# Performance work log

Measured on AMD Instinct MI355X. Metric: run time of the kernel, lower is better.

The kernel has to match this reference:

```python
import jax, jax.numpy as jnp
import numpy as np
import math

DIM = 512
WINDOW = 4
TOPK = 8


def setup_inputs() -> dict:
    key = jax.random.key(0)
    ks = jax.random.split(key, 14)
    B, N, D = 4, 4096, DIM
    s = 0.02
    return {
        'mu':  jax.random.normal(ks[0], (B, N, D), jnp.float32),
        'Wq':  jax.random.normal(ks[1], (D, D), jnp.float32) * s,
        'bq':  jnp.zeros((D,), jnp.float32),
        'Wk':  jax.random.normal(ks[2], (D, D), jnp.float32) * s,
        'bk':  jnp.zeros((D,), jnp.float32),
        'Wv':  jax.random.normal(ks[3], (D, D), jnp.float32) * s,
        'bv':  jnp.zeros((D,), jnp.float32),
        'Wm1': jax.random.normal(ks[4], (2 * D, D), jnp.float32) * s,
        'bm1': jnp.zeros((D,), jnp.float32),
        'Wm2': jax.random.normal(ks[5], (D, D), jnp.float32) * s,
        'bm2': jnp.zeros((D,), jnp.float32),
        'Wo':  jax.random.normal(ks[6], (2 * D, D), jnp.float32) * s,
        'bo':  jnp.zeros((D,), jnp.float32),
    }


def reference(mu, Wq, bq, Wk, bk, Wv, bv, Wm1, bm1, Wm2, bm2, Wo, bo):
    B, N, D = mu.shape
    W = WINDOW
    # ---- local windowed message passing ----
    padded = jnp.pad(mu, ((0, 0), (W, 0), (0, 0)))  # left-pad seq with W zeros
    # neighbors[:, n, w-1] = mu[:, n-w] (zeros if n-w < 0); [B, N, W, D]
    neighbors = jnp.stack([padded[:, W - w:W - w + N, :] for w in range(1, W + 1)], axis=2)
    self_exp = jnp.broadcast_to(mu[:, :, None, :], neighbors.shape)
    h = jnp.concatenate([self_exp, neighbors], axis=-1)  # [B, N, W, 2D]
    h = jax.nn.silu(h @ Wm1 + bm1)
    local_msgs = (h @ Wm2 + bm2).mean(axis=2)  # [B, N, D]
    # ---- sparse causal global attention ----
    q = mu @ Wq + bq
    k = mu @ Wk + bk
    v = mu @ Wv + bv
    scores = jnp.einsum('bnd,bmd->bnm', q, k) * (1.0 / math.sqrt(D))
    causal = jnp.tril(jnp.ones((N, N), bool))
    scores = jnp.where(causal, scores, -jnp.inf)
    # top-k then softmax over kept entries == softmax over scatter(-inf elsewhere)
    topk_vals, topk_idx = jax.lax.top_k(scores, TOPK)  # [B, N, K]
    probs = jax.nn.softmax(topk_vals, axis=-1)
    bi = jnp.arange(B)[:, None, None]
    ni = jnp.arange(N)[None, :, None]
    attn = jnp.zeros_like(scores).at[bi, ni, topk_idx].set(probs)  # [B, N, N]
    global_msgs = jnp.einsum('bnm,bmd->bnd', attn, v)
    return jnp.concatenate([local_msgs, global_msgs], axis=-1) @ Wo + bo
```

## Files before the change

### kernel.cpp

```cpp
#include <hip/hip_runtime.h>
#include <math.h>

#define DIM 512
#define NSEQ 4096
#define BATCH 4
#define ROWS (BATCH * NSEQ)

typedef unsigned long long u64;
typedef unsigned int u32;
typedef unsigned short u16;
typedef __attribute__((ext_vector_type(8))) short bf16x8;
typedef __attribute__((ext_vector_type(4))) float f32x4;

typedef const __attribute__((address_space(1))) void* gas1;
typedef __attribute__((address_space(3))) void* las3;

__device__ __forceinline__ u32 to_bf16(float f) {
  u32 x = __float_as_uint(f);
  return (x + 0x7fffu + ((x >> 16) & 1u)) >> 16;
}
__device__ __forceinline__ u32 pk2(float a, float b) {
  return to_bf16(a) | (to_bf16(b) << 16);
}
__device__ __forceinline__ uint4 pk8(float4 a, float4 b) {
  return make_uint4(pk2(a.x, a.y), pk2(a.z, a.w), pk2(b.x, b.y), pk2(b.z, b.w));
}
__device__ __forceinline__ float bf2f(u32 lo16) {
  return __uint_as_float(lo16 << 16);
}

__device__ __forceinline__ void insert_top8(u64 (&a)[8], u64 key) {
  if (key <= a[7]) return;
  a[7] = key;
#pragma unroll
  for (int i = 7; i > 0; --i) {
    u64 x = a[i - 1], y = a[i];
    u64 hi = x > y ? x : y;
    u64 lo = x > y ? y : x;
    a[i - 1] = hi;
    a[i] = lo;
  }
}
template<int NN>
__device__ __forceinline__ void insert_topN(u64 (&a)[NN], u64 key) {
  if (key <= a[NN - 1]) return;
  a[NN - 1] = key;
#pragma unroll
  for (int i = NN - 1; i > 0; --i) {
    u64 x = a[i - 1], y = a[i];
    u64 hi = x > y ? x : y;
    u64 lo = x > y ? y : x;
    a[i - 1] = hi;
    a[i] = lo;
  }
}
__device__ __forceinline__ float decode_val(u64 key) {
  u32 ord = (u32)(key >> 32);
  u32 s = (ord & 0x80000000u) ? (ord ^ 0x80000000u) : ~ord;
  return __uint_as_float(s);
}
__device__ __forceinline__ u64 pack_key(float v, int m) {
  u32 sb = __float_as_uint(v);
  u32 ord = sb ^ ((sb >> 31) ? 0xFFFFFFFFu : 0x80000000u);
  return ((u64)ord << 32) | (u32)(~(u32)m);
}

__device__ __forceinline__ int fbal(int sub) {
  const int g = sub >> 5, i = sub & 31;
  return (g == 0) ? i : (g == 1) ? (63 - i) : (g == 2) ? (64 + i) : (127 - i);
}

__global__ __launch_bounds__(256) void gemm64qk(const float* __restrict__ mu,
                                                const float* __restrict__ Wq,
                                                const float* __restrict__ bq,
                                                const float* __restrict__ Wk,
                                                const float* __restrict__ bk,
                                                float* __restrict__ Q,
                                                float* __restrict__ Kf,
                                                u16* __restrict__ Kc,
                                                u16* __restrict__ Mu16) {
  __shared__ float As[16][132];
  __shared__ float Bs[16][144];
  const int tid = threadIdx.x;
  const int tx = tid & 15, ty = tid >> 4;
  const int bx = blockIdx.x;
  const bool isK = bx >= 4;
  const int n0 = (bx & 3) * 128;
  const int m0 = blockIdx.y * 128;
  const float* W = isK ? Wk : Wq;
  const float* bias = isK ? bk : bq;
  float* C = isK ? Kf : Q;
  const int arow = tid >> 1, ah8 = (tid & 1) * 8;
  const int bkk = tid >> 4, bslot = tid & 15;
  float acc[8][8] = {};
  for (int k0 = 0; k0 < DIM; k0 += 16) {
    float4 a0 = *(const float4*)(mu + (size_t)(m0 + arow) * DIM + (k0 + ah8));
    float4 a1 = *(const float4*)(mu + (size_t)(m0 + arow) * DIM + (k0 + ah8 + 4));
    float4 b0 = *(const float4*)(W + (size_t)(k0 + bkk) * DIM + (n0 + bslot * 8));
    float4 b1 = *(const float4*)(W + (size_t)(k0 + bkk) * DIM + (n0 + bslot * 8 + 4));
    if (bx == 0)
      *(uint4*)(Mu16 + (size_t)(m0 + arow) * DIM + k0 + ah8) = pk8(a0, a1);
    As[ah8 + 0][arow] = a0.x; As[ah8 + 1][arow] = a0.y;
    As[ah8 + 2][arow] = a0.z; As[ah8 + 3][arow] = a0.w;
    As[ah8 + 4][arow] = a1.x; As[ah8 + 5][arow] = a1.y;
    As[ah8 + 6][arow] = a1.z; As[ah8 + 7][arow] = a1.w;
    *(float4*)&Bs[bkk][bslot * 9] = b0;
    *(float4*)&Bs[bkk][bslot * 9 + 4] = b1;
    __syncthreads();
#pragma unroll
    for (int kk = 0; kk < 16; ++kk) {
      float4 av0 = *(const float4*)&As[kk][ty * 8];
      float4 av1 = *(const float4*)&As[kk][ty * 8 + 4];
      float4 bv0 = *(const float4*)&Bs[kk][tx * 9];
      float4 bv1 = *(const float4*)&Bs[kk][tx * 9 + 4];
      float a8[8] = {av0.x, av0.y, av0.z, av0.w, av1.x, av1.y, av1.z, av1.w};
      float b8[8] = {bv0.x, bv0.y, bv0.z, bv0.w, bv1.x, bv1.y, bv1.z, bv1.w};
#pragma unroll
      for (int i = 0; i < 8; ++i)
#pragma unroll
        for (int j = 0; j < 8; ++j)
          acc[i][j] = fmaf(a8[i], b8[j], acc[i][j]);
    }
    __syncthreads();
  }
  float4 bb0 = *(const float4*)(bias + n0 + tx * 8);
  float4 bb1 = *(const float4*)(bias + n0 + tx * 8 + 4);
#pragma unroll
  for (int i = 0; i < 8; ++i) {
    int row = m0 + ty * 8 + i;
#pragma unroll
    for (int jb = 0; jb < 2; ++jb) {
      int col = n0 + tx * 8 + jb * 4;
      float4 bb = jb ? bb1 : bb0;
      float4 o;
      o.x = acc[i][jb * 4 + 0] + bb.x;
      o.y = acc[i][jb * 4 + 1] + bb.y;
      o.z = acc[i][jb * 4 + 2] + bb.z;
      o.w = acc[i][jb * 4 + 3] + bb.w;
      *(float4*)(C + (size_t)row * DIM + col) = o;
      if (isK) {
        int batch = row >> 12, key = row & 4095;
        int kt = key >> 6, kl = key & 63;
        int chunk = col >> 5;
        size_t didx = ((size_t)batch << 21) +
                      ((size_t)((kt * 16 + chunk) * 64 + kl)) * 32 + (col & 31);
        *(uint2*)(Kc + didx) = make_uint2(pk2(o.x, o.y), pk2(o.z, o.w));
      }
    }
  }
}

__global__ __launch_bounds__(256) void wtrans7(const float* __restrict__ Wv,
                                               const float* __restrict__ Wm1,
                                               const float* __restrict__ Wm2,
                                               const float* __restrict__ Wo,
                                               u16* __restrict__ WT) {
  const size_t DD = (size_t)DIM * DIM;
  const int y = blockIdx.y;
  u16* dst = WT + (size_t)y * DD;
  int o = blockIdx.x * 256 + threadIdx.x;
  if (y == 6) {
    const float* s = Wm2 + (size_t)o * 4;
    ((uint2*)dst)[o] = make_uint2(pk2(s[0], s[1]), pk2(s[2], s[3]));
    return;
  }
  const float* src = (y == 0) ? Wv
                   : (y == 1) ? Wm1
                   : (y == 2) ? Wm1 + DD
                   : (y == 3) ? Wm2
                   : (y == 4) ? Wo
                              : Wo + DD;
  int n = o >> 7;
  int k0 = (o & 127) * 4;
  float a0 = src[(size_t)(k0 + 0) * DIM + n];
  float a1 = src[(size_t)(k0 + 1) * DIM + n];
  float a2 = src[(size_t)(k0 + 2) * DIM + n];
  float a3 = src[(size_t)(k0 + 3) * DIM + n];
  ((uint2*)dst)[(n << 7) + (k0 >> 2)] = make_uint2(pk2(a0, a1), pk2(a2, a3));
}

__global__ __launch_bounds__(256) void wtrans2(const float* __restrict__ Wcombf,
                                               const u16* __restrict__ WoBT,
                                               u16* __restrict__ WT2) {
  int o = blockIdx.x * 256 + threadIdx.x;
  int n = o >> 8;
  int k = (o & 255) * 4;
  if (k < 512) {
    float a0 = Wcombf[(size_t)(k + 0) * DIM + n];
    float a1 = Wcombf[(size_t)(k + 1) * DIM + n];
    float a2 = Wcombf[(size_t)(k + 2) * DIM + n];
    float a3 = Wcombf[(size_t)(k + 3) * DIM + n];
    *(uint2*)&WT2[(size_t)n * 1024 + k] = make_uint2(pk2(a0, a1), pk2(a2, a3));
  } else {
    *(uint2*)&WT2[(size_t)n * 1024 + k] = *(const uint2*)&WoBT[(size_t)n * 512 + (k - 512)];
  }
}

__global__ void bcomb_k(const float* __restrict__ bm2, const float* __restrict__ Wo,
                        const float* __restrict__ bo, float* __restrict__ bc) {
  int c = blockIdx.x * 256 + threadIdx.x;
  if (c >= DIM) return;
  float s = bo[c];
  for (int k = 0; k < DIM; ++k) s = fmaf(bm2[k], Wo[(size_t)k * DIM + c], s);
  bc[c] = s;
}

__global__ __launch_bounds__(256, 4) void gemmbf(const u16* __restrict__ A, int lda,
                                                 const u16* __restrict__ WT, int K,
                                                 const float* __restrict__ bias,
                                                 float* C, int ldc) {
  __shared__ u16 As[128 * 32];
  __shared__ u16 Bs[128 * 32];
  const int tid = threadIdx.x;
  const int n0 = blockIdx.x * 128;
  const int m0 = blockIdx.y * 128;
  const int l = tid & 63, lr = l & 15, lu = l >> 4;
  const int wid = tid >> 6, wr = wid >> 1, wc = wid & 1;
  const int lrow = l >> 2, lseg = (l & 3) * 8;
  f32x4 acc[4][4] = {};
  for (int k0 = 0; k0 < K; k0 += 32) {
    __syncthreads();
#pragma unroll
    for (int j = 0; j < 2; ++j) {
      int r0 = wid * 32 + j * 16;
      const u16* sa = A + (size_t)(m0 + r0 + lrow) * lda + k0 + lseg;
      const u16* sb = WT + (size_t)(n0 + r0 + lrow) * K + k0 + lseg;
      __builtin_amdgcn_global_load_lds((gas1)sa, (las3)&As[r0 * 32], 16, 0, 0);
      __builtin_amdgcn_global_load_lds((gas1)sb, (las3)&Bs[r0 * 32], 16, 0, 0);
    }
    __syncthreads();
    bf16x8 af[4], bf_[4];
#pragma unroll
    for (int fr = 0; fr < 4; ++fr) {
      int row = wr * 64 + fr * 16 + lr;
      af[fr] = *(const bf16x8*)&As[row * 32 + lu * 8];
    }
#pragma unroll
    for (int fc = 0; fc < 4; ++fc) {
      int col = wc * 64 + fc * 16 + lr;
      bf_[fc] = *(const bf16x8*)&Bs[col * 32 + lu * 8];
    }
#pragma unroll
    for (int fr = 0; fr < 4; ++fr)
#pragma unroll
      for (int fc = 0; fc < 4; ++fc)
        acc[fr][fc] = __builtin_amdgcn_mfma_f32_16x16x32_bf16(af[fr], bf_[fc], acc[fr][fc], 0, 0, 0);
  }
#pragma unroll
  for (int fr = 0; fr < 4; ++fr)
#pragma unroll
    for (int fc = 0; fc < 4; ++fc) {
      int col = n0 + wc * 64 + fc * 16 + lr;
      float bb = bias ? bias[col] : 0.f;
#pragma unroll
      for (int j = 0; j < 4; ++j) {
        int row = m0 + wr * 64 + fr * 16 + lu * 4 + j;
        C[(size_t)row * ldc + col] = acc[fr][fc][j] + bb;
      }
    }
}

__global__ __launch_bounds__(256, 4) void gemmbf_b16(const u16* __restrict__ A, int lda,
                                                     const u16* __restrict__ WT, int K,
                                                     const float* __restrict__ bias,
                                                     u16* Cb, int ldc) {
  __shared__ u16 As[128 * 32];
  __shared__ u16 Bs[128 * 32];
  const int tid = threadIdx.x;
  const int n0 = blockIdx.x * 128;
  const int m0 = blockIdx.y * 128;
  const int l = tid & 63, lr = l & 15, lu = l >> 4;
  const int wid = tid >> 6, wr = wid >> 1, wc = wid & 1;
  const int lrow = l >> 2, lseg = (l & 3) * 8;
  f32x4 acc[4][4] = {};
  for (int k0 = 0; k0 < K; k0 += 32) {
    __syncthreads();
#pragma unroll
    for (int j = 0; j < 2; ++j) {
      int r0 = wid * 32 + j * 16;
      const u16* sa = A + (size_t)(m0 + r0 + lrow) * lda + k0 + lseg;
      const u16* sb = WT + (size_t)(n0 + r0 + lrow) * K + k0 + lseg;
      __builtin_amdgcn_global_load_lds((gas1)sa, (las3)&As[r0 * 32], 16, 0, 0);
      __builtin_amdgcn_global_load_lds((gas1)sb, (las3)&Bs[r0 * 32], 16, 0, 0);
    }
    __syncthreads();
    bf16x8 af[4], bf_[4];
#pragma unroll
    for (int fr = 0; fr < 4; ++fr) {
      int row = wr * 64 + fr * 16 + lr;
      af[fr] = *(const bf16x8*)&As[row * 32 + lu * 8];
    }
#pragma unroll
    for (int fc = 0; fc < 4; ++fc) {
      int col = wc * 64 + fc * 16 + lr;
      bf_[fc] = *(const bf16x8*)&Bs[col * 32 + lu * 8];
    }
#pragma unroll
    for (int fr = 0; fr < 4; ++fr)
#pragma unroll
      for (int fc = 0; fc < 4; ++fc)
        acc[fr][fc] = __builtin_amdgcn_mfma_f32_16x16x32_bf16(af[fr], bf_[fc], acc[fr][fc], 0, 0, 0);
  }
#pragma unroll
  for (int fr = 0; fr < 4; ++fr)
#pragma unroll
    for (int fc = 0; fc < 4; ++fc) {
      int col = n0 + wc * 64 + fc * 16 + lr;
      float bb = bias ? bias[col] : 0.f;
#pragma unroll
      for (int j = 0; j < 4; ++j) {
        int row = m0 + wr * 64 + fr * 16 + lu * 4 + j;
        Cb[(size_t)row * ldc + col] = (u16)to_bf16(acc[fr][fc][j] + bb);
      }
    }
}

__global__ __launch_bounds__(256) void silu_combine(const u16* __restrict__ Pair,
                                                    const float* __restrict__ bm1,
                                                    u16* __restrict__ P16) {
  size_t idx = (size_t)blockIdx.x * 256 + threadIdx.x;
  int r = (int)(idx >> 7);
  int c4 = (int)(idx & 127);
  int n = r & (NSEQ - 1);
  uint2 av = *(const uint2*)&Pair[(size_t)r * 1024 + c4 * 4];
  const float4 bm = ((const float4*)bm1)[c4];
  float bx = bf2f(av.x & 0xffffu) + bm.x;
  float by = __uint_as_float(av.x & 0xffff0000u) + bm.y;
  float bz = bf2f(av.y & 0xffffu) + bm.z;
  float bw = __uint_as_float(av.y & 0xffff0000u) + bm.w;
  float sx = 0.f, sy = 0.f, sz = 0.f, sw = 0.f;
#pragma unroll
  for (int w = 1; w <= 4; ++w) {
    float ex = bx, ey = by, ez = bz, ew = bw;
    if (n >= w) {
      uint2 nb = *(const uint2*)&Pair[(size_t)(r - w) * 1024 + 512 + c4 * 4];
      ex += bf2f(nb.x & 0xffffu);
      ey += __uint_as_float(nb.x & 0xffff0000u);
      ez += bf2f(nb.y & 0xffffu);
      ew += __uint_as_float(nb.y & 0xffff0000u);
    }
    sx += ex / (1.f + expf(-ex));
    sy += ey / (1.f + expf(-ey));
    sz += ez / (1.f + expf(-ez));
    sw += ew / (1.f + expf(-ew));
  }
  *(uint2*)(P16 + (size_t)r * 1024 + c4 * 4) =
      make_uint2(pk2(0.25f * sx, 0.25f * sy), pk2(0.25f * sz, 0.25f * sw));
}

__global__ __launch_bounds__(256, 4) void attn_fused(const float* __restrict__ Qf,
                                                     const float* __restrict__ Kf,
                                                     const u16* __restrict__ Kc,
                                                     const u16* __restrict__ V16,
                                                     u16* __restrict__ P16) {
  __shared__ union UA {
    struct { u16 Qs[16 * 512]; u64 cand[256][8]; } s;
    float Qf32[16][512];
  } uA;
  __shared__ int cidx[16][16];
  __shared__ u64 exkey[16][16];
  __shared__ float psm[16][8];
  __shared__ int pidx[16][8];

  const int tid = threadIdx.x;
  const int bid = blockIdx.x;
  const int xcd = bid & 7;
  const int b = xcd >> 1;
  const int par = xcd & 1;
  const int sub = bid >> 3;
  const int qt = 2 * fbal(sub) + par;
  const int n0 = qt * 16;
  const size_t rb = (size_t)b * NSEQ;
  const float SCALE_F = 0.04419417382415922f;

  const int l = tid & 63, lr = l & 15, lu = l >> 4;
  const int wid = tid >> 6;
  const int mbase = lu * 4;

  {
    int row = tid >> 4, part = tid & 15;
    const float4* src = (const float4*)(Qf + ((rb + n0 + row) << 9));
#pragma unroll
    for (int c = 0; c < 4; ++c) {
      int slot = part * 4 + c;
      float4 x = src[slot * 2], y = src[slot * 2 + 1];
      *(uint4*)&uA.s.Qs[row * 512 + (slot ^ (row & 7)) * 8] = pk8(x, y);
    }
  }
  __syncthreads();

  u64 best[8] = {};
  const int nq = n0 + lr;

  const int nkt = (n0 + 16 + 63) >> 6;
  const int lo = (lr * 32) + lu * 8;
  for (int kt = wid; kt < nkt; kt += 4) {
    const int m0 = kt << 6;
    const u16* kb = Kc + ((size_t)b << 21) + (size_t)kt * 32768;
    f32x4 acc[4] = {};
    bf16x8 kcur[4], knxt[4];
#pragma unroll
    for (int fk = 0; fk < 4; ++fk)
      kcur[fk] = *(const bf16x8*)(kb + fk * 512 + lo);
#pragma unroll
    for (int ks = 0; ks < 16; ++ks) {
      if (ks < 15) {
        const u16* cb = kb + (ks + 1) * 2048;
#pragma unroll
        for (int fk = 0; fk < 4; ++fk)
          knxt[fk] = *(const bf16x8*)(cb + fk * 512 + lo);
      }
      bf16x8 qf = *(const bf16x8*)&uA.s.Qs[lr * 512 + ((ks * 4 + lu) ^ (lr & 7)) * 8];
      __builtin_amdgcn_s_setprio(1);
#pragma unroll
      for (int fk = 0; fk < 4; ++fk)
        acc[fk] = __builtin_amdgcn_mfma_f32_16x16x32_bf16(kcur[fk], qf, acc[fk], 0, 0, 0);
      __builtin_amdgcn_s_setprio(0);
      if (ks < 15) {
#pragma unroll
        for (int fk = 0; fk < 4; ++fk) kcur[fk] = knxt[fk];
      }
    }
    if (m0 + 63 <= n0) {
#pragma unroll
      for (int fk = 0; fk < 4; ++fk)
#pragma unroll
        for (int j = 0; j < 4; ++j)
          insert_top8(best, pack_key(acc[fk][j], m0 + fk * 16 + mbase + j));
    } else {
#pragma unroll
      for (int fk = 0; fk < 4; ++fk)
#pragma unroll
        for (int j = 0; j < 4; ++j) {
          int m = m0 + fk * 16 + mbase + j;
          if (m <= nq) insert_top8(best, pack_key(acc[fk][j], m));
        }
    }
  }

  __syncthreads();
#pragma unroll
  for (int i = 0; i < 8; ++i) uA.s.cand[tid][i] = best[i];
  __syncthreads();

  if (tid < 16) {
    u64 mb[16] = {};
    for (int w = 0; w < 4; ++w)
      for (int u = 0; u < 4; ++u) {
        const u64* cl = uA.s.cand[w * 64 + u * 16 + tid];
#pragma unroll
        for (int i = 0; i < 8; ++i) insert_topN<16>(mb, cl[i]);
      }
#pragma unroll
    for (int i = 0; i < 16; ++i)
      cidx[tid][i] = (mb[i] != 0ULL) ? (int)(~(u32)mb[i]) : -1;
  }
  __syncthreads();

  {
    int row = tid >> 4, seg = tid & 15;
    const float4* src = (const float4*)(Qf + ((rb + n0 + row) << 9));
    float4* dst = (float4*)&uA.Qf32[row][0];
#pragma unroll
    for (int c = 0; c < 8; ++c) dst[seg * 8 + c] = src[seg * 8 + c];
  }
  __syncthreads();

  {
    const int g = tid >> 2;
    const int lsub = tid & 3;
    const int qi = g >> 2;
    const int cblk = g & 3;
    const float4* q4 = (const float4*)&uA.Qf32[qi][0];
#pragma unroll
    for (int cc = 0; cc < 4; ++cc) {
      int c = cblk * 4 + cc;
      int ci = cidx[qi][c];
      float4 p = make_float4(0.f, 0.f, 0.f, 0.f);
      if (ci >= 0) {
        const float4* k4 = (const float4*)(Kf + ((rb + ci) << 9));
#pragma unroll 8
        for (int t = 0; t < 32; ++t) {
          float4 kv = k4[4 * t + lsub];
          float4 qv = q4[4 * t + lsub];
          p.x = fmaf(kv.x, qv.x, p.x);
          p.y = fmaf(kv.y, qv.y, p.y);
          p.z = fmaf(kv.z, qv.z, p.z);
          p.w = fmaf(kv.w, qv.w, p.w);
        }
      }
      p.x += __shfl_xor(p.x, 2);
      p.y += __shfl_xor(p.y, 2);
      p.z += __shfl_xor(p.z, 2);
      p.w += __shfl_xor(p.w, 2);
      p.x += __shfl_xor(p.x, 1);
      p.y += __shfl_xor(p.y, 1);
      p.z += __shfl_xor(p.z, 1);
      p.w += __shfl_xor(p.w, 1);
      float rx = p.x + p.z;
      float ry = p.y + p.w;
      float r = rx + ry;
      if (lsub == 0)
        exkey[qi][c] = (ci >= 0) ? pack_key(r * SCALE_F, ci) : 0ULL;
    }
  }
  __syncthreads();

  if (tid < 16) {
    u64 mb[8] = {};
#pragma unroll
    for (int t2 = 0; t2 < 16; ++t2) insert_top8(mb, exkey[tid][t2]);
    float vmax = decode_val(mb[0]);
    float e[8];
#pragma unroll
    for (int i = 0; i < 8; ++i)
      e[i] = (mb[i] != 0ULL) ? expf(decode_val(mb[i]) - vmax) : 0.f;
    float s01 = e[0] + e[1], s23 = e[2] + e[3];
    float s45 = e[4] + e[5], s67 = e[6] + e[7];
    float ssum = (s01 + s23) + (s45 + s67);
#pragma unroll
    for (int i = 0; i < 8; ++i) {
      psm[tid][i] = e[i] / ssum;
      pidx[tid][i] = (mb[i] != 0ULL) ? (int)(~(u32)mb[i]) : 0;
    }
  }
  __syncthreads();

  {
    const int qi = tid >> 4, seg = tid & 15;
    float pp[8];
    int ix[8];
#pragma unroll
    for (int i = 0; i < 8; ++i) { pp[i] = psm[qi][i]; ix[i] = pidx[qi][i]; }
    u16* Gb = P16 + ((size_t)(rb + n0 + qi)) * 1024 + 512 + seg * 32;
#pragma unroll
    for (int it = 0; it < 8; ++it) {
      float4 a = make_float4(0.f, 0.f, 0.f, 0.f);
#pragma unroll
      for (int i = 0; i < 8; ++i) {
        uint2 vv = *(const uint2*)(V16 + ((size_t)(rb + ix[i])) * 512 + seg * 32 + it * 4);
        a.x = fmaf(pp[i], bf2f(vv.x & 0xffffu), a.x);
        a.y = fmaf(pp[i], __uint_as_float(vv.x & 0xffff0000u), a.y);
        a.z = fmaf(pp[i], bf2f(vv.y & 0xffffu), a.z);
        a.w = fmaf(pp[i], __uint_as_float(vv.y & 0xffff0000u), a.w);
      }
      *(uint2*)(Gb + it * 4) = make_uint2(pk2(a.x, a.y), pk2(a.z, a.w));
    }
  }
}

extern "C" void kernel_launch(void* const* d_in, const int* in_sizes, int n_in,
                              void* d_out, int out_size, void* d_ws, size_t ws_size,
                              hipStream_t stream) {
  const float* mu = (const float*)d_in[0];
  const float* Wq = (const float*)d_in[1];
  const float* bq = (const float*)d_in[2];
  const float* Wk = (const float*)d_in[3];
  const float* bk = (const float*)d_in[4];
  const float* Wv = (const float*)d_in[5];
  const float* bv = (const float*)d_in[6];
  const float* Wm1 = (const float*)d_in[7];
  const float* bm1 = (const float*)d_in[8];
  const float* Wm2 = (const float*)d_in[9];
  const float* bm2 = (const float*)d_in[10];
  const float* Wo = (const float*)d_in[11];
  const float* bo = (const float*)d_in[12];
  float* out = (float*)d_out;

  float* ws = (float*)d_ws;
  const size_t RD = (size_t)ROWS * DIM;
  const size_t DD = (size_t)DIM * DIM;
  float* X1 = ws;
  float* X2 = X1 + RD;
  u16* P16 = (u16*)(X2 + RD);
  u16* Pair = P16 + RD * 2;
  u16* V16 = Pair + RD * 2;
  u16* Kc = V16 + RD;
  u16* WT = Kc + RD;
  u16* WvT = WT;
  u16* Wm1aT = WT + DD;
  u16* WoTT = WT + 4 * DD;
  u16* WoBT = WT + 5 * DD;
  u16* Wm216 = WT + 6 * DD;
  u16* WT2 = WT + 7 * DD;
  float* Wcombf = (float*)(WT2 + (size_t)512 * 1024);
  float* bcomb = Wcombf + DD;
  u16* Mu16 = (u16*)(bcomb + 512);

  dim3 blk(256);
  dim3 gqk(8, ROWS / 128);
  dim3 gbf(DIM / 128, ROWS / 128);
  dim3 gbf2(2 * DIM / 128, ROWS / 128);

  wtrans7<<<dim3(256, 7), blk, 0, stream>>>(Wv, Wm1, Wm2, Wo, WT);
  gemmbf<<<dim3(4, 4), blk, 0, stream>>>(Wm216, 512, WoTT, 512, (const float*)nullptr, Wcombf, 512);
  bcomb_k<<<dim3(2), blk, 0, stream>>>(bm2, Wo, bo, bcomb);
  wtrans2<<<dim3(512), blk, 0, stream>>>(Wcombf, WoBT, WT2);

  gemm64qk<<<gqk, blk, 0, stream>>>(mu, Wq, bq, Wk, bk, X1, X2, Kc, Mu16);

  gemmbf_b16<<<gbf, blk, 0, stream>>>(Mu16, 512, WvT, 512, bv, V16, 512);

  attn_fused<<<dim3(1024), blk, 0, stream>>>(X1, X2, Kc, V16, P16);

  gemmbf_b16<<<gbf2, blk, 0, stream>>>(Mu16, 512, Wm1aT, 512, (const float*)nullptr, Pair, 1024);
  silu_combine<<<dim3(ROWS * 128 / 256), blk, 0, stream>>>(Pair, bm1, P16);

  gemmbf<<<dim3(4, 128), blk, 0, stream>>>(P16, 1024, WT2, 1024, bcomb, out, 512);
}
```

Baseline: 635.1 us.

## Pre-transpose mu and double-buffer QK GEMM with direct global-to-LDS loads

Adds a transpose kernel that writes mu in column-major fp32 form and emits the bf16 copy, taking that work out of the QK GEMM. The fp32 QK GEMM then uses global_load_lds to fill double-buffered LDS tiles, so the next k-tile loads while the current one is computed, replacing register staging and scattered LDS stores. This costs an extra pass over mu (a 32 MB read and a 32 MB write) and extra workspace. The LDS padding is removed, which may add bank conflicts.

New measurement: 635.1 us. No clear change (-0.0%).

```diff
diff --git a/kernel.cpp b/kernel.cpp
--- a/kernel.cpp
+++ b/kernel.cpp
@@ -70,17 +70,35 @@
   return (g == 0) ? i : (g == 1) ? (63 - i) : (g == 2) ? (64 + i) : (127 - i);
 }
 
-__global__ __launch_bounds__(256) void gemm64qk(const float* __restrict__ mu,
+__global__ __launch_bounds__(256) void mutrans(const float* __restrict__ mu,
+                                               float* __restrict__ muT,
+                                               u16* __restrict__ Mu16) {
+  __shared__ float t[32][33];
+  const int kb = blockIdx.x * 32;
+  const int rb = blockIdx.y * 32;
+  const int tx = threadIdx.x & 31, ty = threadIdx.x >> 5;
+#pragma unroll
+  for (int i = 0; i < 32; i += 8) {
+    float v = mu[(size_t)(rb + ty + i) * DIM + kb + tx];
+    t[ty + i][tx] = v;
+    Mu16[(size_t)(rb + ty + i) * DIM + kb + tx] = (u16)to_bf16(v);
+  }
+  __syncthreads();
+#pragma unroll
+  for (int i = 0; i < 32; i += 8)
+    muT[(size_t)(kb + ty + i) * ROWS + rb + tx] = t[tx][ty + i];
+}
+
+__global__ __launch_bounds__(256) void gemm64qk(const float* __restrict__ muT,
                                                 const float* __restrict__ Wq,
                                                 const float* __restrict__ bq,
                                                 const float* __restrict__ Wk,
                                                 const float* __restrict__ bk,
                                                 float* __restrict__ Q,
                                                 float* __restrict__ Kf,
-                                                u16* __restrict__ Kc,
-                                                u16* __restrict__ Mu16) {
-  __shared__ float As[16][132];
-  __shared__ float Bs[16][144];
+                                                u16* __restrict__ Kc) {
+  __shared__ float As[2][16][128];
+  __shared__ float Bs[2][16][128];
   const int tid = threadIdx.x;
   const int tx = tid & 15, ty = tid >> 4;
   const int bx = blockIdx.x;
@@ -90,29 +108,34 @@
   const float* W = isK ? Wk : Wq;
   const float* bias = isK ? bk : bq;
   float* C = isK ? Kf : Q;
-  const int arow = tid >> 1, ah8 = (tid & 1) * 8;
-  const int bkk = tid >> 4, bslot = tid & 15;
+  const int wid = tid >> 6, l = tid & 63;
+  const int lrow = l >> 5;
+  const int lcol = (l & 31) * 4;
+
+#define QK_STAGE(buf, k0)                                                      \
+  {                                                                            \
+    _Pragma("unroll")                                                          \
+    for (int j = 0; j < 2; ++j) {                                              \
+      int kk0 = wid * 4 + j * 2;                                               \
+      const float* sa = muT + (size_t)((k0) + kk0 + lrow) * ROWS + m0 + lcol;  \
+      const float* sb = W + (size_t)((k0) + kk0 + lrow) * DIM + n0 + lcol;     \
+      __builtin_amdgcn_global_load_lds((gas1)sa, (las3)&As[buf][kk0][0], 16, 0, 0); \
+      __builtin_amdgcn_global_load_lds((gas1)sb, (las3)&Bs[buf][kk0][0], 16, 0, 0); \
+    }                                                                          \
+  }
+
   float acc[8][8] = {};
-  for (int k0 = 0; k0 < DIM; k0 += 16) {
-    float4 a0 = *(const float4*)(mu + (size_t)(m0 + arow) * DIM + (k0 + ah8));
-    float4 a1 = *(const float4*)(mu + (size_t)(m0 + arow) * DIM + (k0 + ah8 + 4));
-    float4 b0 = *(const float4*)(W + (size_t)(k0 + bkk) * DIM + (n0 + bslot * 8));
-    float4 b1 = *(const float4*)(W + (size_t)(k0 + bkk) * DIM + (n0 + bslot * 8 + 4));
-    if (bx == 0)
-      *(uint4*)(Mu16 + (size_t)(m0 + arow) * DIM + k0 + ah8) = pk8(a0, a1);
-    As[ah8 + 0][arow] = a0.x; As[ah8 + 1][arow] = a0.y;
-    As[ah8 + 2][arow] = a0.z; As[ah8 + 3][arow] = a0.w;
-    As[ah8 + 4][arow] = a1.x; As[ah8 + 5][arow] = a1.y;
-    As[ah8 + 6][arow] = a1.z; As[ah8 + 7][arow] = a1.w;
-    *(float4*)&Bs[bkk][bslot * 9] = b0;
-    *(float4*)&Bs[bkk][bslot * 9 + 4] = b1;
-    __syncthreads();
+  QK_STAGE(0, 0);
+  __syncthreads();
+  for (int t = 0; t < 32; ++t) {
+    const int buf = t & 1;
+    if (t < 31) QK_STAGE(buf ^ 1, (t + 1) * 16);
 #pragma unroll
     for (int kk = 0; kk < 16; ++kk) {
-      float4 av0 = *(const float4*)&As[kk][ty * 8];
-      float4 av1 = *(const float4*)&As[kk][ty * 8 + 4];
-      float4 bv0 = *(const float4*)&Bs[kk][tx * 9];
-      float4 bv1 = *(const float4*)&Bs[kk][tx * 9 + 4];
+      float4 av0 = *(const float4*)&As[buf][kk][ty * 8];
+      float4 av1 = *(const float4*)&As[buf][kk][ty * 8 + 4];
+      float4 bv0 = *(const float4*)&Bs[buf][kk][tx * 8];
+      float4 bv1 = *(const float4*)&Bs[buf][kk][tx * 8 + 4];
       float a8[8] = {av0.x, av0.y, av0.z, av0.w, av1.x, av1.y, av1.z, av1.w};
       float b8[8] = {bv0.x, bv0.y, bv0.z, bv0.w, bv1.x, bv1.y, bv1.z, bv1.w};
 #pragma unroll
@@ -123,6 +146,8 @@
     }
     __syncthreads();
   }
+#undef QK_STAGE
+
   float4 bb0 = *(const float4*)(bias + n0 + tx * 8);
   float4 bb1 = *(const float4*)(bias + n0 + tx * 8 + 4);
 #pragma unroll
@@ -586,6 +611,7 @@
   float* Wcombf = (float*)(WT2 + (size_t)512 * 1024);
   float* bcomb = Wcombf + DD;
   u16* Mu16 = (u16*)(bcomb + 512);
+  float* MuT = (float*)(Mu16 + RD);
 
   dim3 blk(256);
   dim3 gqk(8, ROWS / 128);
@@ -597,7 +623,9 @@
   bcomb_k<<<dim3(2), blk, 0, stream>>>(bm2, Wo, bo, bcomb);
   wtrans2<<<dim3(512), blk, 0, stream>>>(Wcombf, WoBT, WT2);
 
-  gemm64qk<<<gqk, blk, 0, stream>>>(mu, Wq, bq, Wk, bk, X1, X2, Kc, Mu16);
+  mutrans<<<dim3(DIM / 32, ROWS / 32), blk, 0, stream>>>(mu, MuT, Mu16);
+
+  gemm64qk<<<gqk, blk, 0, stream>>>(MuT, Wq, bq, Wk, bk, X1, X2, Kc);
 
   gemmbf_b16<<<gbf, blk, 0, stream>>>(Mu16, 512, WvT, 512, bv, V16, 512);
 
```
